# Performance work log

Measured on AMD Instinct MI355X. Metric: run time of the kernel, lower is better.

## Reference

```python
import jax, jax.numpy as jnp
import numpy as np

TEMPERATURE = 2.0 / 3.0
LIMIT_A = -0.1
LIMIT_B = 1.1

N_NODES = 50000
N_CLUSTERS = 64
N_RELATIONS = 8
N_EDGES = 1000000


def setup_inputs() -> dict:
    key = jax.random.key(0)
    ks = jax.random.split(key, 6)
    xavier = float(np.sqrt(6.0 / (N_CLUSTERS + N_CLUSTERS)))
    return {
        "assignments": jax.random.normal(ks[0], (N_NODES, N_CLUSTERS), jnp.float32),
        "inter_cluster_logits": jax.random.uniform(ks[1], (N_RELATIONS, N_CLUSTERS, N_CLUSTERS), jnp.float32, -xavier, xavier),
        "log_alpha": jnp.zeros((N_RELATIONS, N_CLUSTERS, N_CLUSTERS), jnp.float32),
        "absent_bias": jnp.zeros((N_RELATIONS,), jnp.float32),
        "edge_index": jax.random.randint(ks[2], (2, N_EDGES), 0, N_NODES, jnp.int32),
        "edge_type": jax.random.randint(ks[3], (N_EDGES,), 0, N_RELATIONS, jnp.int32),
        "neg_edge_index": jax.random.randint(ks[4], (2, N_EDGES), 0, N_NODES, jnp.int32),
        "neg_edge_type": jax.random.randint(ks[5], (N_EDGES,), 0, N_RELATIONS, jnp.int32),
    }


def _edge_logits(assignments, weights, absent_bias, edge_index, edge_type):
    # src, dst: [E, C] gathers (irregular access)
    src = assignments[edge_index[0]]
    dst = assignments[edge_index[1]]
    n_rel = weights.shape[0]
    # torch.bmm(W[et], dst[:, :, None]) == dst @ W[et].T ; compute per relation
    # (fixed small relation loop; avoids materializing [E, C, C]) then select.
    logits_all = jnp.stack(
        [jnp.sum(src * (dst @ weights[r].T), axis=-1) for r in range(n_rel)],
        axis=-1,
    )  # [E, R]
    logits = jnp.take_along_axis(logits_all, edge_type[:, None], axis=1)[:, 0]
    return logits + absent_bias[edge_type]


def reference(assignments, inter_cluster_logits, log_alpha, absent_bias,
              edge_index, edge_type, neg_edge_index, neg_edge_type):
    # Hard-concrete gate, eval mode: z = clamp(sigmoid(log_alpha)*(b-a)+a, 0, 1)
    gate = jnp.clip(jax.nn.sigmoid(log_alpha) * (LIMIT_B - LIMIT_A) + LIMIT_A, 0.0, 1.0)
    weights = jax.nn.sigmoid(inter_cluster_logits) * gate  # [R, C, C]

    pos_logits = _edge_logits(assignments, weights, absent_bias, edge_index, edge_type)
    neg_logits = _edge_logits(assignments, weights, absent_bias, neg_edge_index, neg_edge_type)

    # BCE-with-logits: target=1 -> softplus(-x); target=0 -> softplus(x)
    pos_loss = jnp.mean(jax.nn.softplus(-pos_logits))
    neg_loss = jnp.mean(jax.nn.softplus(neg_logits))
    return pos_loss + neg_loss
```

## Files before the change

### kernel.cpp

```cpp
#include <hip/hip_runtime.h>
#include <hip/hip_bf16.h>
#include <math.h>

#define E_EDGES 1000000
#define N_NODES 50000
#define N_C     64
#define N_REL   8
#define CHB     1024
#define CAP     192
#define NBLK    977
#define BT      256
#define SENT    0xFFFFFFFFu

typedef __attribute__((ext_vector_type(4))) float floatx4;
typedef __attribute__((ext_vector_type(2))) float floatx2;

static __device__ __forceinline__ unsigned pk4_fp8(float a, float b, float c, float d) {
    unsigned w = 0;
    w = __builtin_amdgcn_cvt_pk_fp8_f32(a, b, w, false);
    w = __builtin_amdgcn_cvt_pk_fp8_f32(c, d, w, true);
    return w;
}

static __device__ __forceinline__ long long pack64(unsigned lo, unsigned hi) {
    uint2 u; u.x = lo; u.y = hi;
    return __builtin_bit_cast(long long, u);
}

__global__ __launch_bounds__(256) void prep_kernel(
    const float* __restrict__ assign,
    const float* __restrict__ icl,
    const float* __restrict__ la,
    unsigned char* __restrict__ Wp8,
    unsigned char* __restrict__ AS8,
    float* __restrict__ out)
{
    int tid = blockIdx.x * blockDim.x + threadIdx.x;
    int nth = gridDim.x * blockDim.x;
    if (tid == 0) out[0] = 0.0f;

    for (int idx = tid; idx < N_REL * N_C * 16; idx += nth) {
        int row = idx >> 4, dq = idx & 15;
        int q = dq >> 2, c = (dq >> 1) & 1, jh = dq & 1;
        int k0 = (2 * c + jh) * 16 + 4 * q;
        float wv[4];
        #pragma unroll
        for (int b = 0; b < 4; ++b) {
            int srci = (row << 6) + k0 + b;
            float w = 1.0f / (1.0f + __expf(-icl[srci]));
            float g = 1.0f / (1.0f + __expf(-la[srci])) * 1.2f - 0.1f;
            g = fminf(fmaxf(g, 0.0f), 1.0f);
            wv[b] = w * g;
        }
        ((unsigned*)Wp8)[idx] = pk4_fp8(wv[0], wv[1], wv[2], wv[3]);
    }

    for (int n = tid; n < N_NODES; n += nth) {
        const float4* a4 = (const float4*)(assign + (size_t)n * N_C);
        unsigned w[16];
        #pragma unroll
        for (int i = 0; i < 16; ++i) {
            float4 v = a4[i];
            w[i] = pk4_fp8(v.x, v.y, v.z, v.w);
        }
        uint4* as = (uint4*)(AS8 + (size_t)n * N_C);
        #pragma unroll
        for (int q = 0; q < 4; ++q) {
            uint4 o;
            o.x = w[0 * 4 + q];
            o.y = w[1 * 4 + q];
            o.z = w[2 * 4 + q];
            o.w = w[3 * 4 + q];
            as[q] = o;
        }
    }
}

__global__ __launch_bounds__(BT, 5) void edge_kernel(
    const unsigned char* __restrict__ AS8,
    const unsigned char* __restrict__ Wp8,
    const float* __restrict__ absent_bias,
    const int* __restrict__ ei, const int* __restrict__ et,
    const int* __restrict__ nei, const int* __restrict__ net,
    float* __restrict__ out)
{
    __shared__ unsigned list[N_REL * CAP];
    __shared__ unsigned cnt[N_REL];
    __shared__ float red[4];
    if (threadIdx.x < N_REL) cnt[threadIdx.x] = 0u;
    __syncthreads();

    int blk = blockIdx.x;
    bool isneg = blk >= NBLK;
    int lb = isneg ? blk - NBLK : blk;
    const int* Es = isneg ? nei : ei;
    const int* Et = isneg ? net : et;
    float sign = isneg ? 1.0f : -1.0f;
    int base = lb * CHB;
    int elim = min(base + CHB, E_EDGES);

    {
        int e0 = base + threadIdx.x;
        int sv[4], dv[4], rv[4];
        bool mv[4];
        #pragma unroll
        for (int k = 0; k < 4; ++k) {
            int e = e0 + k * BT;
            mv[k] = e < elim;
            int ec = mv[k] ? e : base;
            sv[k] = __builtin_nontemporal_load(&Es[ec]);
            dv[k] = __builtin_nontemporal_load(&Es[E_EDGES + ec]);
            rv[k] = __builtin_nontemporal_load(&Et[ec]);
        }
        #pragma unroll
        for (int k = 0; k < 4; ++k) {
            if (mv[k]) {
                unsigned rank = atomicAdd(&cnt[rv[k]], 1u);
                if (rank < CAP)
                    list[rv[k] * CAP + rank] = (unsigned)sv[k] | ((unsigned)dv[k] << 16);
            }
        }
    }
    __syncthreads();

    if (threadIdx.x < N_REL * 16) {
        int r = threadIdx.x >> 4;
        int i = threadIdx.x & 15;
        int n = min((int)cnt[r], CAP);
        int padded = ((n + 15) >> 4) << 4;
        int slot = n + i;
        if (slot < padded) list[r * CAP + slot] = SENT;
    }
    __syncthreads();

    int lane = threadIdx.x & 63;
    int wid  = __builtin_amdgcn_readfirstlane(threadIdx.x >> 6);
    int n16  = lane & 15;
    int quad = lane >> 4;
    float loss = 0.0f;

    int G0 = __builtin_amdgcn_readfirstlane((min((int)cnt[0], CAP) + 15) >> 4);
    int G1 = __builtin_amdgcn_readfirstlane((min((int)cnt[1], CAP) + 15) >> 4);
    int G2 = __builtin_amdgcn_readfirstlane((min((int)cnt[2], CAP) + 15) >> 4);
    int G3 = __builtin_amdgcn_readfirstlane((min((int)cnt[3], CAP) + 15) >> 4);
    int G4 = __builtin_amdgcn_readfirstlane((min((int)cnt[4], CAP) + 15) >> 4);
    int G5 = __builtin_amdgcn_readfirstlane((min((int)cnt[5], CAP) + 15) >> 4);
    int G6 = __builtin_amdgcn_readfirstlane((min((int)cnt[6], CAP) + 15) >> 4);
    int G7 = __builtin_amdgcn_readfirstlane((min((int)cnt[7], CAP) + 15) >> 4);
    int go1 = G0;
    int go2 = go1 + G1;
    int go3 = go2 + G2;
    int go4 = go3 + G3;
    int go5 = go4 + G4;
    int go6 = go5 + G5;
    int go7 = go6 + G6;
    int tg  = go7 + G7;

    #define LOCATE(ITEM, R, GOF)                                   \
        do {                                                       \
            R = 0; GOF = 0;                                        \
            if ((ITEM) >= go1) { R = 1; GOF = go1; }               \
            if ((ITEM) >= go2) { R = 2; GOF = go2; }               \
            if ((ITEM) >= go3) { R = 3; GOF = go3; }               \
            if ((ITEM) >= go4) { R = 4; GOF = go4; }               \
            if ((ITEM) >= go5) { R = 5; GOF = go5; }               \
            if ((ITEM) >= go6) { R = 6; GOF = go6; }               \
            if ((ITEM) >= go7) { R = 7; GOF = go7; }               \
        } while (0)

    #define RECF(ITEM, R, RECV)                                    \
        do {                                                       \
            int gof_;                                               \
            LOCATE(ITEM, R, gof_);                                  \
            RECV = list[R * CAP + ((ITEM) - gof_) * 16 + n16];      \
        } while (0)

    #define GISS(RECV, SREG, DREG)                                           \
        do {                                                                 \
            unsigned sm_ = (RECV) != SENT ? ((RECV) & 0xFFFFu) : 0u;         \
            unsigned dm_ = (RECV) != SENT ? ((RECV) >> 16) : 0u;             \
            SREG = *(const uint4*)(AS8 + ((size_t)sm_ << 6) + quad * 16);    \
            DREG = *(const uint4*)(AS8 + ((size_t)dm_ << 6) + quad * 16);    \
        } while (0)

    int start = (wid * tg) >> 2;
    int end   = ((wid + 1) * tg) >> 2;

    int rC = 0, rG = 0, rR = 0;
    unsigned recC = SENT, recG = SENT, recR = SENT;
    uint4 SC = {0,0,0,0}, DC = {0,0,0,0}, SG = {0,0,0,0}, DG = {0,0,0,0};
    uint4 wfm[4];
    float bias = 0.0f;
    const floatx4 zero4 = {0.0f, 0.0f, 0.0f, 0.0f};

    if (start < end) {
        RECF(start, rC, recC);
        GISS(recC, SC, DC);
        #pragma unroll
        for (int mt = 0; mt < 4; ++mt)
            wfm[mt] = *(const uint4*)(Wp8 + ((rC * 64 + mt * 16 + n16) << 6) + quad * 16);
        bias = absent_bias[rC];
        if (start + 1 < end) { RECF(start + 1, rG, recG); GISS(recG, SG, DG); }
        if (start + 2 < end) { RECF(start + 2, rR, recR); }
    }

    for (int it = start; it < end; ++it) {
        int rN = 0;
        unsigned recN = SENT;
        if (it + 3 < end) RECF(it + 3, rN, recN);

        uint4 SN = {0,0,0,0}, DN = {0,0,0,0};
        if (it + 2 < end) GISS(recR, SN, DN);

        long long bD0 = pack64(DC.x, DC.y);
        long long bD1 = pack64(DC.z, DC.w);
        unsigned sw[4] = {SC.x, SC.y, SC.z, SC.w};
        float d0 = 0.0f, d1 = 0.0f;
        #pragma unroll
        for (int gidx = 0; gidx < 2; ++gidx) {
            const int ma = 2 * gidx, mb = 2 * gidx + 1;
            floatx4 p0 = zero4, p1 = zero4;
            p0 = __builtin_amdgcn_mfma_f32_16x16x32_fp8_fp8(
                    pack64(wfm[ma].x, wfm[ma].y), bD0, p0, 0, 0, 0);
            p1 = __builtin_amdgcn_mfma_f32_16x16x32_fp8_fp8(
                    pack64(wfm[mb].x, wfm[mb].y), bD0, p1, 0, 0, 0);
            p0 = __builtin_amdgcn_mfma_f32_16x16x32_fp8_fp8(
                    pack64(wfm[ma].z, wfm[ma].w), bD1, p0, 0, 0, 0);
            p1 = __builtin_amdgcn_mfma_f32_16x16x32_fp8_fp8(
                    pack64(wfm[mb].z, wfm[mb].w), bD1, p1, 0, 0, 0);
            floatx2 lo0 = __builtin_amdgcn_cvt_pk_f32_fp8((int)sw[ma], false);
            floatx2 hi0 = __builtin_amdgcn_cvt_pk_f32_fp8((int)sw[ma], true);
            floatx2 lo1 = __builtin_amdgcn_cvt_pk_f32_fp8((int)sw[mb], false);
            floatx2 hi1 = __builtin_amdgcn_cvt_pk_f32_fp8((int)sw[mb], true);
            d0 = fmaf(lo0.x, p0[0], d0);
            d1 = fmaf(lo1.x, p1[0], d1);
            d0 = fmaf(lo0.y, p0[1], d0);
            d1 = fmaf(lo1.y, p1[1], d1);
            d0 = fmaf(hi0.x, p0[2], d0);
            d1 = fmaf(hi1.x, p1[2], d1);
            d0 = fmaf(hi0.y, p0[3], d0);
            d1 = fmaf(hi1.y, p1[3], d1);
        }
        float dot = d0 + d1;
        dot += __shfl_xor(dot, 16);
        dot += __shfl_xor(dot, 32);
        if (quad == 0 && recC != SENT) {
            float x = sign * (dot + bias);
            loss += fmaxf(x, 0.0f) + __logf(1.0f + __expf(-fabsf(x)));
        }

        if (rG != rC) {
            #pragma unroll
            for (int mt = 0; mt < 4; ++mt)
                wfm[mt] = *(const uint4*)(Wp8 + ((rG * 64 + mt * 16 + n16) << 6) + quad * 16);
            bias = absent_bias[rG];
        }
        rC = rG; recC = recG; SC = SG; DC = DG;
        rG = rR; recG = recR; SG = SN; DG = DN;
        rR = rN; recR = recN;
    }

    loss += __shfl_xor(loss, 1);
    loss += __shfl_xor(loss, 2);
    loss += __shfl_xor(loss, 4);
    loss += __shfl_xor(loss, 8);
    loss += __shfl_xor(loss, 16);
    loss += __shfl_xor(loss, 32);
    if (lane == 0) red[wid] = loss;
    __syncthreads();
    if (threadIdx.x == 0) {
        float t = red[0] + red[1] + red[2] + red[3];
        atomicAdd(out, t * (1.0f / (float)E_EDGES));
    }
}

extern "C" void kernel_launch(void* const* d_in, const int* in_sizes, int n_in,
                              void* d_out, int out_size, void* d_ws, size_t ws_size,
                              hipStream_t stream) {
    const float* assign = (const float*)d_in[0];
    const float* icl    = (const float*)d_in[1];
    const float* la     = (const float*)d_in[2];
    const float* ab     = (const float*)d_in[3];
    const int*   ei     = (const int*)d_in[4];
    const int*   et     = (const int*)d_in[5];
    const int*   nei    = (const int*)d_in[6];
    const int*   net    = (const int*)d_in[7];
    float* out = (float*)d_out;

    char* basep = (char*)d_ws;
    unsigned char* Wp8 = (unsigned char*)basep;
    unsigned char* AS8 = (unsigned char*)(basep + 65536);

    prep_kernel<<<256, 256, 0, stream>>>(assign, icl, la, Wp8, AS8, out);
    edge_kernel<<<2 * NBLK, BT, 0, stream>>>(AS8, Wp8, ab, ei, et, nei, net, out);
}
```

Measured before the change: 134.9 us.

## Restructure gather pipeline into three-slot rotating buffers unrolled by three

Replaces the shift-register prefetch pipeline (index fetch three ahead, gather two ahead) with three fixed register slots, each issuing its index and row gathers together. The loop is manually unrolled by three so no register copies are needed between iterations, and the weight reload is tracked by the last loaded relation. The goal is to cut the register moves and branch overhead per edge group while keeping two gathers in flight. In exchange, index fetch and gather are now serialized within each slot, and the unrolled body uses more registers.

Result: no change. 134.4 us (-0.4%).

```diff
diff --git a/kernel.cpp b/kernel.cpp
--- a/kernel.cpp
+++ b/kernel.cpp
@@ -168,96 +168,129 @@
             if ((ITEM) >= go7) { R = 7; GOF = go7; }               \
         } while (0)
 
-    #define RECF(ITEM, R, RECV)                                    \
-        do {                                                       \
-            int gof_;                                               \
-            LOCATE(ITEM, R, gof_);                                  \
-            RECV = list[R * CAP + ((ITEM) - gof_) * 16 + n16];      \
+    #define ISSUE(VIT, RREG, RECV, SREG, DREG)                               \
+        do {                                                                 \
+            if ((VIT) < end) {                                               \
+                int gof_;                                                    \
+                LOCATE(VIT, RREG, gof_);                                     \
+                RECV = list[RREG * CAP + ((VIT) - gof_) * 16 + n16];         \
+                unsigned sm_ = RECV != SENT ? (RECV & 0xFFFFu) : 0u;         \
+                unsigned dm_ = RECV != SENT ? (RECV >> 16) : 0u;             \
+                SREG = *(const uint4*)(AS8 + ((size_t)sm_ << 6) + quad * 16);\
+                DREG = *(const uint4*)(AS8 + ((size_t)dm_ << 6) + quad * 16);\
+            } else {                                                         \
+                RECV = SENT;                                                 \
+            }                                                                \
         } while (0)
 
-    #define GISS(RECV, SREG, DREG)                                           \
+    #define RELOADW(RREG)                                                    \
         do {                                                                 \
-            unsigned sm_ = (RECV) != SENT ? ((RECV) & 0xFFFFu) : 0u;         \
-            unsigned dm_ = (RECV) != SENT ? ((RECV) >> 16) : 0u;             \
-            SREG = *(const uint4*)(AS8 + ((size_t)sm_ << 6) + quad * 16);    \
-            DREG = *(const uint4*)(AS8 + ((size_t)dm_ << 6) + quad * 16);    \
+            if ((RREG) != rW) {                                              \
+                rW = (RREG);                                                 \
+                _Pragma("unroll")                                            \
+                for (int mt = 0; mt < 4; ++mt)                               \
+                    wfm[mt] = *(const uint4*)(Wp8 +                          \
+                        ((rW * 64 + mt * 16 + n16) << 6) + quad * 16);       \
+                bias = absent_bias[rW];                                      \
+            }                                                                \
+        } while (0)
+
+    #define COMPUTE(RECV, SS, DD)                                            \
+        do {                                                                 \
+            long long bD0 = pack64((DD).x, (DD).y);                          \
+            long long bD1 = pack64((DD).z, (DD).w);                          \
+            unsigned sw0 = (SS).x, sw1 = (SS).y, sw2 = (SS).z, sw3 = (SS).w; \
+            float d0 = 0.0f, d1 = 0.0f;                                      \
+            {                                                                \
+                floatx4 p0 = zero4, p1 = zero4;                              \
+                p0 = __builtin_amdgcn_mfma_f32_16x16x32_fp8_fp8(             \
+                        pack64(wfm[0].x, wfm[0].y), bD0, p0, 0, 0, 0);       \
+                p1 = __builtin_amdgcn_mfma_f32_16x16x32_fp8_fp8(             \
+                        pack64(wfm[1].x, wfm[1].y), bD0, p1, 0, 0, 0);       \
+                p0 = __builtin_amdgcn_mfma_f32_16x16x32_fp8_fp8(             \
+                        pack64(wfm[0].z, wfm[0].w), bD1, p0, 0, 0, 0);       \
+                p1 = __builtin_amdgcn_mfma_f32_16x16x32_fp8_fp8(             \
+                        pack64(wfm[1].z, wfm[1].w), bD1, p1, 0, 0, 0);       \
+                floatx2 lo0 = __builtin_amdgcn_cvt_pk_f32_fp8((int)sw0, false);\
+                floatx2 hi0 = __builtin_amdgcn_cvt_pk_f32_fp8((int)sw0, true);\
+                floatx2 lo1 = __builtin_amdgcn_cvt_pk_f32_fp8((int)sw1, false);\
+                floatx2 hi1 = __builtin_amdgcn_cvt_pk_f32_fp8((int)sw1, true);\
+                d0 = fmaf(lo0.x, p0[0], d0); d1 = fmaf(lo1.x, p1[0], d1);    \
+                d0 = fmaf(lo0.y, p0[1], d0); d1 = fmaf(lo1.y, p1[1], d1);    \
+                d0 = fmaf(hi0.x, p0[2], d0); d1 = fmaf(hi1.x, p1[2], d1);    \
+                d0 = fmaf(hi0.y, p0[3], d0); d1 = fmaf(hi1.y, p1[3], d1);    \
+            }                                                                \
+            {                                                                \
+                floatx4 p0 = zero4, p1 = zero4;                              \
+                p0 = __builtin_amdgcn_mfma_f32_16x16x32_fp8_fp8(             \
+                        pack64(wfm[2].x, wfm[2].y), bD0, p0, 0, 0, 0);       \
+                p1 = __builtin_amdgcn_mfma_f32_16x16x32_fp8_fp8(             \
+                        pack64(wfm[3].x, wfm[3].y), bD0, p1, 0, 0, 0);       \
+                p0 = __builtin_amdgcn_mfma_f32_16x16x32_fp8_fp8(             \
+                        pack64(wfm[2].z, wfm[2].w), bD1, p0, 0, 0, 0);       \
+                p1 = __builtin_amdgcn_mfma_f32_16x16x32_fp8_fp8(             \
+                        pack64(wfm[3].z, wfm[3].w), bD1, p1, 0, 0, 0);       \
+                floatx2 lo0 = __builtin_amdgcn_cvt_pk_f32_fp8((int)sw2, false);\
+                floatx2 hi0 = __builtin_amdgcn_cvt_pk_f32_fp8((int)sw2, true);\
+                floatx2 lo1 = __builtin_amdgcn_cvt_pk_f32_fp8((int)sw3, false);\
+                floatx2 hi1 = __builtin_amdgcn_cvt_pk_f32_fp8((int)sw3, true);\
+                d0 = fmaf(lo0.x, p0[0], d0); d1 = fmaf(lo1.x, p1[0], d1);    \
+                d0 = fmaf(lo0.y, p0[1], d0); d1 = fmaf(lo1.y, p1[1], d1);    \
+                d0 = fmaf(hi0.x, p0[2], d0); d1 = fmaf(hi1.x, p1[2], d1);    \
+                d0 = fmaf(hi0.y, p0[3], d0); d1 = fmaf(hi1.y, p1[3], d1);    \
+            }                                                                \
+            float dot = d0 + d1;                                             \
+            dot += __shfl_xor(dot, 16);                                      \
+            dot += __shfl_xor(dot, 32);                                      \
+            float x = sign * (dot + bias);                                   \
+            float sp = fmaxf(x, 0.0f) + __logf(1.0f + __expf(-fabsf(x)));    \
+            bool live = (quad == 0) && (RECV != SENT);                       \
+            loss += live ? sp : 0.0f;                                        \
         } while (0)
 
     int start = (wid * tg) >> 2;
     int end   = ((wid + 1) * tg) >> 2;
 
-    int rC = 0, rG = 0, rR = 0;
-    unsigned recC = SENT, recG = SENT, recR = SENT;
-    uint4 SC = {0,0,0,0}, DC = {0,0,0,0}, SG = {0,0,0,0}, DG = {0,0,0,0};
     uint4 wfm[4];
     float bias = 0.0f;
+    int rW = -1;
     const floatx4 zero4 = {0.0f, 0.0f, 0.0f, 0.0f};
 
     if (start < end) {
-        RECF(start, rC, recC);
-        GISS(recC, SC, DC);
-        #pragma unroll
-        for (int mt = 0; mt < 4; ++mt)
-            wfm[mt] = *(const uint4*)(Wp8 + ((rC * 64 + mt * 16 + n16) << 6) + quad * 16);
-        bias = absent_bias[rC];
-        if (start + 1 < end) { RECF(start + 1, rG, recG); GISS(recG, SG, DG); }
-        if (start + 2 < end) { RECF(start + 2, rR, recR); }
-    }
-
-    for (int it = start; it < end; ++it) {
-        int rN = 0;
-        unsigned recN = SENT;
-        if (it + 3 < end) RECF(it + 3, rN, recN);
-
-        uint4 SN = {0,0,0,0}, DN = {0,0,0,0};
-        if (it + 2 < end) GISS(recR, SN, DN);
-
-        long long bD0 = pack64(DC.x, DC.y);
-        long long bD1 = pack64(DC.z, DC.w);
-        unsigned sw[4] = {SC.x, SC.y, SC.z, SC.w};
-        float d0 = 0.0f, d1 = 0.0f;
-        #pragma unroll
-        for (int gidx = 0; gidx < 2; ++gidx) {
-            const int ma = 2 * gidx, mb = 2 * gidx + 1;
-            floatx4 p0 = zero4, p1 = zero4;
-            p0 = __builtin_amdgcn_mfma_f32_16x16x32_fp8_fp8(
-                    pack64(wfm[ma].x, wfm[ma].y), bD0, p0, 0, 0, 0);
-            p1 = __builtin_amdgcn_mfma_f32_16x16x32_fp8_fp8(
-                    pack64(wfm[mb].x, wfm[mb].y), bD0, p1, 0, 0, 0);
-            p0 = __builtin_amdgcn_mfma_f32_16x16x32_fp8_fp8(
-                    pack64(wfm[ma].z, wfm[ma].w), bD1, p0, 0, 0, 0);
-            p1 = __builtin_amdgcn_mfma_f32_16x16x32_fp8_fp8(
-                    pack64(wfm[mb].z, wfm[mb].w), bD1, p1, 0, 0, 0);
-            floatx2 lo0 = __builtin_amdgcn_cvt_pk_f32_fp8((int)sw[ma], false);
-            floatx2 hi0 = __builtin_amdgcn_cvt_pk_f32_fp8((int)sw[ma], true);
-            floatx2 lo1 = __builtin_amdgcn_cvt_pk_f32_fp8((int)sw[mb], false);
-            floatx2 hi1 = __builtin_amdgcn_cvt_pk_f32_fp8((int)sw[mb], true);
-            d0 = fmaf(lo0.x, p0[0], d0);
-            d1 = fmaf(lo1.x, p1[0], d1);
-            d0 = fmaf(lo0.y, p0[1], d0);
-            d1 = fmaf(lo1.y, p1[1], d1);
-            d0 = fmaf(hi0.x, p0[2], d0);
-            d1 = fmaf(hi1.x, p1[2], d1);
-            d0 = fmaf(hi0.y, p0[3], d0);
-            d1 = fmaf(hi1.y, p1[3], d1);
-        }
-        float dot = d0 + d1;
-        dot += __shfl_xor(dot, 16);
-        dot += __shfl_xor(dot, 32);
-        if (quad == 0 && recC != SENT) {
-            float x = sign * (dot + bias);
-            loss += fmaxf(x, 0.0f) + __logf(1.0f + __expf(-fabsf(x)));
-        }
-
-        if (rG != rC) {
-            #pragma unroll
-            for (int mt = 0; mt < 4; ++mt)
-                wfm[mt] = *(const uint4*)(Wp8 + ((rG * 64 + mt * 16 + n16) << 6) + quad * 16);
-            bias = absent_bias[rG];
-        }
-        rC = rG; recC = recG; SC = SG; DC = DG;
-        rG = rR; recG = recR; SG = SN; DG = DN;
-        rR = rN; recR = recN;
+        int rA = 0, rB = 0, rC = 0;
+        unsigned recA, recB, recC;
+        uint4 SA = {0,0,0,0}, DA = {0,0,0,0};
+        uint4 SB = {0,0,0,0}, DB = {0,0,0,0};
+        uint4 SC = {0,0,0,0}, DC = {0,0,0,0};
+
+        int vA = start, vB = start + 1, vC = start + 2;
+        ISSUE(vA, rA, recA, SA, DA);
+        ISSUE(vB, rB, recB, SB, DB);
+        ISSUE(vC, rC, recC, SC, DC);
+        RELOADW(rA);
+
+        int n3 = (end - start + 2) / 3;
+        #pragma clang loop unroll(disable)
+        for (int k = 0; k < n3; ++k) {
+            COMPUTE(recA, SA, DA);
+            vA += 3;
+            int rAn = rA;
+            ISSUE(vA, rAn, recA, SA, DA);
+            RELOADW(rB);
+
+            COMPUTE(recB, SB, DB);
+            vB += 3;
+            int rBn = rB;
+            ISSUE(vB, rBn, recB, SB, DB);
+            RELOADW(rC);
+
+            COMPUTE(recC, SC, DC);
+            vC += 3;
+            int rCn = rC;
+            ISSUE(vC, rCn, recC, SC, DC);
+            rA = rAn; rB = rBn; rC = rCn;
+            RELOADW(rA);
+        }
     }
 
     loss += __shfl_xor(loss, 1);
```
